# Kernel tuning notes

Hardware: AMD Instinct MI355X
Metric: run time of the kernel (lower is better)

Reference implementation:

```python
import jax, jax.numpy as jnp
import numpy as np

B, S, H, NH = 2, 2048, 1024, 16
DH = H // NH
FF = 4 * H
EPS = 1e-5


def setup_inputs() -> dict:
    key = jax.random.key(0)
    ks = jax.random.split(key, 16)
    sd = 0.02
    inp = {
        "x": jax.random.normal(ks[0], (B, S, H), dtype=jnp.float32),
        "Wq": jax.random.normal(ks[1], (H, H), dtype=jnp.float32) * sd,
        "bq": jnp.zeros((H,), jnp.float32),
        "Wk": jax.random.normal(ks[2], (H, H), dtype=jnp.float32) * sd,
        "bk": jnp.zeros((H,), jnp.float32),
        "Wv": jax.random.normal(ks[3], (H, H), dtype=jnp.float32) * sd,
        "bv": jnp.zeros((H,), jnp.float32),
        "Wo": jax.random.normal(ks[4], (H, H), dtype=jnp.float32) * sd,
        "bo": jnp.zeros((H,), jnp.float32),
        "W1": jax.random.normal(ks[5], (H, FF), dtype=jnp.float32) * sd,
        "b1": jnp.zeros((FF,), jnp.float32),
        "W2": jax.random.normal(ks[6], (FF, H), dtype=jnp.float32) * sd,
        "b2": jnp.zeros((H,), jnp.float32),
        "g1": jnp.ones((H,), jnp.float32),
        "be1": jnp.zeros((H,), jnp.float32),
        "g2": jnp.ones((H,), jnp.float32),
        "be2": jnp.zeros((H,), jnp.float32),
    }
    return inp


def _layernorm(x, g, b):
    mu = jnp.mean(x, axis=-1, keepdims=True)
    var = jnp.mean(jnp.square(x - mu), axis=-1, keepdims=True)
    return (x - mu) * jax.lax.rsqrt(var + EPS) * g + b


def _block(x, Wq, bq, Wk, bk, Wv, bv, Wo, bo, W1, b1, W2, b2, g1, be1, g2, be2):
    # pre-LN attention
    h = _layernorm(x, g1, be1)
    q = (h @ Wq + bq).reshape(B, S, NH, DH)
    k = (h @ Wk + bk).reshape(B, S, NH, DH)
    v = (h @ Wv + bv).reshape(B, S, NH, DH)
    scale = DH ** -0.5
    scores = jnp.einsum("bqhd,bkhd->bhqk", q, k) * scale  # [B,NH,S,S]
    causal = jnp.tril(jnp.ones((S, S), dtype=bool))
    scores = jnp.where(causal, scores, -jnp.inf)
    attn = jax.nn.softmax(scores, axis=-1)
    out = jnp.einsum("bhqk,bkhd->bqhd", attn, v).reshape(B, S, H)
    x = x + (out @ Wo + bo)
    # pre-LN FFN with exact GELU (torch nn.GELU default)
    h = _layernorm(x, g2, be2)
    h = jax.nn.gelu(h @ W1 + b1, approximate=False)
    return x + (h @ W2 + b2)


def reference(x, Wq, bq, Wk, bk, Wv, bv, Wo, bo, W1, b1, W2, b2, g1, be1, g2, be2):
    return _block(x, Wq, bq, Wk, bk, Wv, bv, Wo, bo, W1, b1, W2, b2, g1, be1, g2, be2)
```

## Files before the change

### kernel.cpp

```cpp
#include <hip/hip_runtime.h>
#include <cstdint>
#include <cstddef>

typedef unsigned short u16;
typedef __attribute__((ext_vector_type(8))) __bf16 bf16v8;
typedef __attribute__((ext_vector_type(8))) unsigned short u16x8;
typedef __attribute__((ext_vector_type(4))) float f32x4;

constexpr int Bc = 2, Sc = 2048, Hc = 1024, NHc = 16, DHc = 64, FFc = 4096;
constexpr int Mc = Bc * Sc;

__device__ __forceinline__ u16 f2bf(float f) {
  unsigned u = __builtin_bit_cast(unsigned, f);
  return (u16)((u + 0x7FFFu + ((u >> 16) & 1u)) >> 16);
}

__device__ __forceinline__ void gload_lds16(const void* g, void* l) {
  __builtin_amdgcn_global_load_lds(
      (const __attribute__((address_space(1))) unsigned*)(uintptr_t)g,
      (__attribute__((address_space(3))) unsigned*)(unsigned)(uintptr_t)l,
      16, 0, 0);
}

__global__ __launch_bounds__(256) void wconv_kernel(const float* __restrict__ W,
                                                    u16* __restrict__ Wt, int K, int N) {
  __shared__ float tile[64][65];
  const int n0 = blockIdx.x << 6, k0 = blockIdx.y << 6;
  const int t = threadIdx.x;
  const int col = t & 63, r0 = t >> 6;
#pragma unroll
  for (int i = 0; i < 16; ++i) {
    int r = (i << 2) + r0;
    tile[r][col] = W[(size_t)(k0 + r) * N + n0 + col];
  }
  __syncthreads();
#pragma unroll
  for (int i = 0; i < 16; ++i) {
    int n = (i << 2) + r0;
    Wt[(size_t)(n0 + n) * K + k0 + col] = f2bf(tile[col][n]);
  }
}

__global__ __launch_bounds__(256) void ln_kernel(const float* __restrict__ x,
                                                 const float* __restrict__ g,
                                                 const float* __restrict__ be,
                                                 u16* __restrict__ y) {
  const int row = blockIdx.x;
  const int t = threadIdx.x;
  const float4 v = ((const float4*)(x + (size_t)row * Hc))[t];
  float s1 = v.x + v.y + v.z + v.w;
  float s2 = v.x * v.x + v.y * v.y + v.z * v.z + v.w * v.w;
#pragma unroll
  for (int o = 32; o > 0; o >>= 1) {
    s1 += __shfl_xor(s1, o);
    s2 += __shfl_xor(s2, o);
  }
  __shared__ float r1[4], r2[4];
  const int wave = t >> 6, lane = t & 63;
  if (lane == 0) { r1[wave] = s1; r2[wave] = s2; }
  __syncthreads();
  s1 = r1[0] + r1[1] + r1[2] + r1[3];
  s2 = r2[0] + r2[1] + r2[2] + r2[3];
  const float mu = s1 * (1.f / Hc);
  const float var = s2 * (1.f / Hc) - mu * mu;
  const float rs = rsqrtf(var + 1e-5f);
  const float4 gv = ((const float4*)g)[t];
  const float4 bv = ((const float4*)be)[t];
  ushort4 ov;
  ov.x = f2bf((v.x - mu) * rs * gv.x + bv.x);
  ov.y = f2bf((v.y - mu) * rs * gv.y + bv.y);
  ov.z = f2bf((v.z - mu) * rs * gv.z + bv.z);
  ov.w = f2bf((v.w - mu) * rs * gv.w + bv.w);
  ((ushort4*)(y + (size_t)row * Hc))[t] = ov;
}

template <int EPI>
__global__ __launch_bounds__(256, 2) void gemm_kernel(
    const u16* __restrict__ A, const u16* __restrict__ Bt,
    const float* __restrict__ bias, const float* __restrict__ res,
    u16* __restrict__ outb, float* __restrict__ outf, float* __restrict__ outf2,
    int N, int Kext, int lda, int ldb, int koff) {
  __shared__ __align__(16) char smraw[32768];
  u16 (*As)[128][32] = (u16(*)[128][32])smraw;
  u16 (*Bs)[128][32] = (u16(*)[128][32])(smraw + 16384);
  float (*Cs)[16][132] = (float(*)[16][132])smraw;

  const int t = threadIdx.x;
  const int wave = t >> 6, lane = t & 63;
  const int bm = blockIdx.y, bn = blockIdx.x;
  const int kz = blockIdx.z;
  A += (size_t)kz * koff;
  Bt += (size_t)kz * koff;
  const int wm = wave >> 1, wn = wave & 1;
  const int fr = lane & 15, fk = (lane >> 4) << 3;

  f32x4 acc[4][4] = {};

  const int srow = (wave << 4) + (lane >> 2);
  const int scol = (lane & 3) << 3;
  const u16* Ag0 = A + (size_t)(bm * 128 + srow) * lda + scol;
  const u16* Ag1 = Ag0 + (size_t)64 * lda;
  const u16* Bg0 = Bt + (size_t)(bn * 128 + srow) * ldb + scol;
  const u16* Bg1 = Bg0 + (size_t)64 * ldb;

  const int nk = Kext >> 5;
  auto STAGE = [&](int buf, int k0) {
    gload_lds16(Ag0 + k0, &As[buf][wave << 4][0]);
    gload_lds16(Ag1 + k0, &As[buf][64 + (wave << 4)][0]);
    gload_lds16(Bg0 + k0, &Bs[buf][wave << 4][0]);
    gload_lds16(Bg1 + k0, &Bs[buf][64 + (wave << 4)][0]);
  };

  STAGE(0, 0);
  asm volatile("s_waitcnt vmcnt(0)" ::: "memory");
  __syncthreads();
  int cur = 0;
  for (int kt = 0; kt < nk; ++kt) {
    if (kt + 1 < nk) STAGE(cur ^ 1, (kt + 1) << 5);
    bf16v8 af[4], bfr[4];
#pragma unroll
    for (int i = 0; i < 4; ++i) af[i] = *(const bf16v8*)&As[cur][(wm << 6) + (i << 4) + fr][fk];
#pragma unroll
    for (int j = 0; j < 4; ++j) bfr[j] = *(const bf16v8*)&Bs[cur][(wn << 6) + (j << 4) + fr][fk];
#pragma unroll
    for (int i = 0; i < 4; ++i)
#pragma unroll
      for (int j = 0; j < 4; ++j)
        acc[i][j] = __builtin_amdgcn_mfma_f32_16x16x32_bf16(af[i], bfr[j], acc[i][j], 0, 0, 0);
    asm volatile("s_waitcnt vmcnt(0)" ::: "memory");
    __syncthreads();
    cur ^= 1;
  }

  const int cr = (lane >> 4) << 2, cc = lane & 15;
  const int b2 = t >> 7, u = t & 127, lr = u >> 3, c0 = (u & 7) << 4;
  float* fdst = (EPI == 3 && kz) ? outf2 : outf;

  for (int i = 0; i < 4; ++i) {
#pragma unroll
    for (int j = 0; j < 4; ++j) {
      int col = (wn << 6) + (j << 4) + cc;
      float bz = 0.f;
      if constexpr (EPI != 3) bz = bias[(bn << 7) + col];
#pragma unroll
      for (int r = 0; r < 4; ++r) Cs[wm][cr + r][col] = acc[i][j][r] + bz;
    }
    __syncthreads();
    {
      const float* crow = &Cs[b2][lr][c0];
      f32x4 v0 = *(const f32x4*)(crow);
      f32x4 v1 = *(const f32x4*)(crow + 4);
      f32x4 v2 = *(const f32x4*)(crow + 8);
      f32x4 v3 = *(const f32x4*)(crow + 12);
      const int grow = (bm << 7) + (b2 << 6) + (i << 4) + lr;
      const int gc = (bn << 7) + c0;
      const size_t base = (size_t)grow * N + gc;
      if constexpr (EPI == 0 || EPI == 1) {
        float vv[16];
#pragma unroll
        for (int k = 0; k < 4; ++k) { vv[k] = v0[k]; vv[4 + k] = v1[k]; vv[8 + k] = v2[k]; vv[12 + k] = v3[k]; }
        if constexpr (EPI == 1) {
#pragma unroll
          for (int k = 0; k < 16; ++k)
            vv[k] = 0.5f * vv[k] * (1.0f + erff(vv[k] * 0.70710678118654752f));
        }
        u16x8 o0, o1;
#pragma unroll
        for (int k = 0; k < 8; ++k) { o0[k] = f2bf(vv[k]); o1[k] = f2bf(vv[8 + k]); }
        *(u16x8*)&outb[base] = o0;
        *(u16x8*)&outb[base + 8] = o1;
      } else {
        if constexpr (EPI == 2) {
          const f32x4* rp = (const f32x4*)&res[base];
          v0 += rp[0]; v1 += rp[1]; v2 += rp[2]; v3 += rp[3];
        }
        f32x4* op = (f32x4*)&fdst[base];
        op[0] = v0; op[1] = v1; op[2] = v2; op[3] = v3;
      }
    }
    __syncthreads();
  }
}

__global__ __launch_bounds__(256, 2) void qkv_gemm_kernel(
    const u16* __restrict__ A, const u16* __restrict__ Bt,
    const float* __restrict__ bq, const float* __restrict__ bk,
    const float* __restrict__ bv,
    u16* __restrict__ Qb, u16* __restrict__ Kb, u16* __restrict__ Vtg) {
  constexpr int K = 1024;
  __shared__ __align__(16) char smraw[32768];
  u16 (*As)[128][32] = (u16(*)[128][32])smraw;
  u16 (*Bs)[128][32] = (u16(*)[128][32])(smraw + 16384);
  float (*Cs)[16][132] = (float(*)[16][132])smraw;

  const int t = threadIdx.x;
  const int wave = t >> 6, lane = t & 63;
  const int bm = blockIdx.y, bn = blockIdx.x;
  const int wm = wave >> 1, wn = wave & 1;
  const int fr = lane & 15, fk = (lane >> 4) << 3;
  const int seg = bn >> 3;

  f32x4 acc[4][4] = {};

  const int srow = (wave << 4) + (lane >> 2);
  const int scol = (lane & 3) << 3;
  const u16* Ag0 = A + (size_t)(bm * 128 + srow) * K + scol;
  const u16* Ag1 = Ag0 + (size_t)64 * K;
  const u16* Bg0 = Bt + (size_t)(bn * 128 + srow) * K + scol;
  const u16* Bg1 = Bg0 + (size_t)64 * K;

  const int nk = K >> 5;
  auto STAGE = [&](int buf, int k0) {
    gload_lds16(Ag0 + k0, &As[buf][wave << 4][0]);
    gload_lds16(Ag1 + k0, &As[buf][64 + (wave << 4)][0]);
    gload_lds16(Bg0 + k0, &Bs[buf][wave << 4][0]);
    gload_lds16(Bg1 + k0, &Bs[buf][64 + (wave << 4)][0]);
  };

  STAGE(0, 0);
  asm volatile("s_waitcnt vmcnt(0)" ::: "memory");
  __syncthreads();
  int cur = 0;
  for (int kt = 0; kt < nk; ++kt) {
    if (kt + 1 < nk) STAGE(cur ^ 1, (kt + 1) << 5);
    bf16v8 af[4], bfr[4];
#pragma unroll
    for (int i = 0; i < 4; ++i) af[i] = *(const bf16v8*)&As[cur][(wm << 6) + (i << 4) + fr][fk];
#pragma unroll
    for (int j = 0; j < 4; ++j) bfr[j] = *(const bf16v8*)&Bs[cur][(wn << 6) + (j << 4) + fr][fk];
#pragma unroll
    for (int i = 0; i < 4; ++i)
#pragma unroll
      for (int j = 0; j < 4; ++j)
        acc[i][j] = __builtin_amdgcn_mfma_f32_16x16x32_bf16(af[i], bfr[j], acc[i][j], 0, 0, 0);
    asm volatile("s_waitcnt vmcnt(0)" ::: "memory");
    __syncthreads();
    cur ^= 1;
  }

  const int cr = (lane >> 4) << 2, cc = lane & 15;
  const int b2 = t >> 7, u = t & 127, lr = u >> 3, c0 = (u & 7) << 4;
  const float* bp = (seg == 0) ? bq : (seg == 1) ? bk : bv;

  for (int i = 0; i < 4; ++i) {
#pragma unroll
    for (int j = 0; j < 4; ++j) {
      int col = (wn << 6) + (j << 4) + cc;
      float bz = bp[((bn << 7) + col) & 1023];
#pragma unroll
      for (int r = 0; r < 4; ++r) Cs[wm][cr + r][col] = acc[i][j][r] + bz;
    }
    __syncthreads();
    if (seg < 2) {
      const float* crow = &Cs[b2][lr][c0];
      f32x4 v0 = *(const f32x4*)(crow);
      f32x4 v1 = *(const f32x4*)(crow + 4);
      f32x4 v2 = *(const f32x4*)(crow + 8);
      f32x4 v3 = *(const f32x4*)(crow + 12);
      const int grow = (bm << 7) + (b2 << 6) + (i << 4) + lr;
      const int cn0 = (((bn & 7) << 7) + c0);
      u16* dst = (seg == 0) ? Qb : Kb;
      u16x8 o0, o1;
#pragma unroll
      for (int k = 0; k < 4; ++k) {
        o0[k] = f2bf(v0[k]); o0[4 + k] = f2bf(v1[k]);
        o1[k] = f2bf(v2[k]); o1[4 + k] = f2bf(v3[k]);
      }
      *(u16x8*)&dst[(size_t)grow * 1024 + cn0] = o0;
      *(u16x8*)&dst[(size_t)grow * 1024 + cn0 + 8] = o1;
    } else {
      const int cv = ((bn & 7) << 7) + u;
      const int h = cv >> 6, dh = cv & 63;
#pragma unroll
      for (int oct = 0; oct < 2; ++oct) {
        u16x8 o;
#pragma unroll
        for (int k = 0; k < 8; ++k) o[k] = f2bf(Cs[b2][(oct << 3) + k][u]);
        const int srow2 = (bm << 7) + (b2 << 6) + (i << 4) + (oct << 3);
        const int bb = srow2 >> 11, s = srow2 & 2047;
        size_t idx = ((size_t)(bb * 16 + h)) * (64 * 2048) + (size_t)dh * 2048 + s;
        *(u16x8*)&Vtg[idx] = o;
      }
    }
    __syncthreads();
  }
}

__global__ __launch_bounds__(256) void combine_kernel(float* __restrict__ out,
                                                      const float* __restrict__ p0,
                                                      const float* __restrict__ p1,
                                                      const float* __restrict__ bias) {
  const int i = blockIdx.x * 256 + threadIdx.x;
  f32x4 o = ((f32x4*)out)[i];
  f32x4 a = ((const f32x4*)p0)[i];
  f32x4 b = ((const f32x4*)p1)[i];
  const int col = (i << 2) & 1023;
  f32x4 bb = *(const f32x4*)&bias[col];
  o += a + b + bb;
  ((f32x4*)out)[i] = o;
}

__global__ __launch_bounds__(256, 2) void attn_kernel(const u16* __restrict__ Q,
                                                      const u16* __restrict__ Kb,
                                                      const u16* __restrict__ Vt,
                                                      u16* __restrict__ O) {
  constexpr float LOG2E = 1.4426950408889634f;
  const int bh = blockIdx.y;
  const int t = threadIdx.x, wave = t >> 6, lane = t & 63;
  const int fr = lane & 15, fk = (lane >> 4) << 3;

  __shared__ u16 Ks[64][72];
  __shared__ u16 Vs[64][72];
  __shared__ u16 Ps[4][16][72];

  const size_t base = ((size_t)(bh >> 4) * Sc) * Hc + (bh & 15) * DHc;
  const u16* Qp = Q + base;
  const u16* Kp = Kb + base;
  const u16* Vp = Vt + (size_t)bh * (64 * 2048);

  for (int half = 0; half < 2; ++half) {
    const int qt = half ? (31 - blockIdx.x) : blockIdx.x;
    const int q0 = qt << 6;

    const int qrow = q0 + (wave << 4) + fr;
    const bf16v8 qf0 = *(const bf16v8*)&Qp[(size_t)qrow * Hc + fk];
    const bf16v8 qf1 = *(const bf16v8*)&Qp[(size_t)qrow * Hc + 32 + fk];

    float m[4], l[4];
    f32x4 oacc[4] = {};
#pragma unroll
    for (int r = 0; r < 4; ++r) { m[r] = -INFINITY; l[r] = 0.f; }

    const int crow0 = q0 + (wave << 4) + ((lane >> 4) << 2);

    for (int kv0 = 0; kv0 < q0 + 64; kv0 += 64) {
      __syncthreads();
#pragma unroll
      for (int i = 0; i < 2; ++i) {
        int c = t + (i << 8);
        int r = c >> 3, co = (c & 7) << 3;
        *(u16x8*)&Ks[r][co] = *(const u16x8*)&Kp[(size_t)(kv0 + r) * Hc + co];
        *(u16x8*)&Vs[r][co] = *(const u16x8*)&Vp[(size_t)r * 2048 + kv0 + co];
      }
      __syncthreads();

      f32x4 sc[4];
#pragma unroll
      for (int c = 0; c < 4; ++c) {
        bf16v8 kf0 = *(const bf16v8*)&Ks[(c << 4) + fr][fk];
        bf16v8 kf1 = *(const bf16v8*)&Ks[(c << 4) + fr][32 + fk];
        f32x4 a = {0.f, 0.f, 0.f, 0.f};
        a = __builtin_amdgcn_mfma_f32_16x16x32_bf16(qf0, kf0, a, 0, 0, 0);
        a = __builtin_amdgcn_mfma_f32_16x16x32_bf16(qf1, kf1, a, 0, 0, 0);
        sc[c] = a;
      }
#pragma unroll
      for (int c = 0; c < 4; ++c)
#pragma unroll
        for (int r = 0; r < 4; ++r) sc[c][r] *= 0.125f;
      if (kv0 + 64 > q0) {
#pragma unroll
        for (int c = 0; c < 4; ++c)
#pragma unroll
          for (int r = 0; r < 4; ++r) {
            int kv = kv0 + (c << 4) + fr;
            if (kv > crow0 + r) sc[c][r] = -INFINITY;
          }
      }
      float pm[4];
#pragma unroll
      for (int r = 0; r < 4; ++r)
        pm[r] = fmaxf(fmaxf(sc[0][r], sc[1][r]), fmaxf(sc[2][r], sc[3][r]));
#pragma unroll
      for (int o = 1; o < 16; o <<= 1)
#pragma unroll
        for (int r = 0; r < 4; ++r) pm[r] = fmaxf(pm[r], __shfl_xor(pm[r], o));
      float alpha[4];
#pragma unroll
      for (int r = 0; r < 4; ++r) {
        float mn = fmaxf(m[r], pm[r]);
        alpha[r] = exp2f((m[r] - mn) * LOG2E);
        m[r] = mn;
      }
      float ps[4] = {0.f, 0.f, 0.f, 0.f};
#pragma unroll
      for (int c = 0; c < 4; ++c)
#pragma unroll
        for (int r = 0; r < 4; ++r) {
          float p = exp2f((sc[c][r] - m[r]) * LOG2E);
          sc[c][r] = p;
          ps[r] += p;
        }
#pragma unroll
      for (int o = 1; o < 16; o <<= 1)
#pragma unroll
        for (int r = 0; r < 4; ++r) ps[r] += __shfl_xor(ps[r], o);
#pragma unroll
      for (int r = 0; r < 4; ++r) l[r] = l[r] * alpha[r] + ps[r];

#pragma unroll
      for (int c = 0; c < 4; ++c)
#pragma unroll
        for (int r = 0; r < 4; ++r)
          Ps[wave][((lane >> 4) << 2) + r][(c << 4) + fr] = f2bf(sc[c][r]);
#pragma unroll
      for (int f = 0; f < 4; ++f)
#pragma unroll
        for (int r = 0; r < 4; ++r) oacc[f][r] *= alpha[r];

      const bf16v8 pa0 = *(const bf16v8*)&Ps[wave][fr][fk];
      const bf16v8 pa1 = *(const bf16v8*)&Ps[wave][fr][32 + fk];
#pragma unroll
      for (int f = 0; f < 4; ++f) {
        bf16v8 vf0 = *(const bf16v8*)&Vs[(f << 4) + fr][fk];
        bf16v8 vf1 = *(const bf16v8*)&Vs[(f << 4) + fr][32 + fk];
        oacc[f] = __builtin_amdgcn_mfma_f32_16x16x32_bf16(pa0, vf0, oacc[f], 0, 0, 0);
        oacc[f] = __builtin_amdgcn_mfma_f32_16x16x32_bf16(pa1, vf1, oacc[f], 0, 0, 0);
      }
    }
#pragma unroll
    for (int r = 0; r < 4; ++r) {
      float inv = 1.0f / l[r];
      int row = crow0 + r;
#pragma unroll
      for (int f = 0; f < 4; ++f)
        O[base + (size_t)row * Hc + (f << 4) + fr] = f2bf(oacc[f][r] * inv);
    }
    __syncthreads();
  }
}

extern "C" void kernel_launch(void* const* d_in, const int* in_sizes, int n_in,
                              void* d_out, int out_size, void* d_ws, size_t ws_size,
                              hipStream_t stream) {
  const float* x  = (const float*)d_in[0];
  const float* Wq = (const float*)d_in[1];
  const float* bq = (const float*)d_in[2];
  const float* Wk = (const float*)d_in[3];
  const float* bk = (const float*)d_in[4];
  const float* Wv = (const float*)d_in[5];
  const float* bv = (const float*)d_in[6];
  const float* Wo = (const float*)d_in[7];
  const float* bo = (const float*)d_in[8];
  const float* W1 = (const float*)d_in[9];
  const float* b1 = (const float*)d_in[10];
  const float* W2 = (const float*)d_in[11];
  const float* b2 = (const float*)d_in[12];
  const float* g1 = (const float*)d_in[13];
  const float* be1 = (const float*)d_in[14];
  const float* g2 = (const float*)d_in[15];
  const float* be2 = (const float*)d_in[16];
  float* out = (float*)d_out;

  char* ws = (char*)d_ws;
  const size_t MB = 1024 * 1024;
  u16* wqkv = (u16*)(ws + 0 * MB);
  u16* wo   = (u16*)(ws + 6 * MB);
  u16* w1   = (u16*)(ws + 8 * MB);
  u16* w2   = (u16*)(ws + 16 * MB);
  u16* lnb  = (u16*)(ws + 24 * MB);
  u16* Qb   = (u16*)(ws + 32 * MB);
  u16* Kb   = (u16*)(ws + 40 * MB);
  u16* Vtg  = (u16*)(ws + 48 * MB);
  u16* Ob   = (u16*)(ws + 56 * MB);
  u16* H1   = (u16*)(ws + 32 * MB);
  float* p0 = (float*)(ws + 64 * MB);
  float* p1 = (float*)(ws + 0 * MB);

  dim3 blk(256);
  wconv_kernel<<<dim3(16, 16), blk, 0, stream>>>(Wq, wqkv, 1024, 1024);
  wconv_kernel<<<dim3(16, 16), blk, 0, stream>>>(Wk, wqkv + (size_t)1024 * 1024, 1024, 1024);
  wconv_kernel<<<dim3(16, 16), blk, 0, stream>>>(Wv, wqkv + (size_t)2048 * 1024, 1024, 1024);
  wconv_kernel<<<dim3(16, 16), blk, 0, stream>>>(Wo, wo, 1024, 1024);
  wconv_kernel<<<dim3(64, 16), blk, 0, stream>>>(W1, w1, 1024, 4096);
  wconv_kernel<<<dim3(16, 64), blk, 0, stream>>>(W2, w2, 4096, 1024);

  ln_kernel<<<Mc, blk, 0, stream>>>(x, g1, be1, lnb);

  qkv_gemm_kernel<<<dim3(24, 32), blk, 0, stream>>>(lnb, wqkv, bq, bk, bv, Qb, Kb, Vtg);

  attn_kernel<<<dim3(16, 32), blk, 0, stream>>>(Qb, Kb, Vtg, Ob);

  gemm_kernel<2><<<dim3(8, 32), blk, 0, stream>>>(Ob, wo, bo, x, nullptr, out, nullptr,
                                                  1024, 1024, 1024, 1024, 0);

  ln_kernel<<<Mc, blk, 0, stream>>>(out, g2, be2, lnb);

  gemm_kernel<1><<<dim3(32, 32), blk, 0, stream>>>(lnb, w1, b1, nullptr, H1, nullptr, nullptr,
                                                   4096, 1024, 1024, 1024, 0);

  gemm_kernel<3><<<dim3(8, 32, 2), blk, 0, stream>>>(H1, w2, nullptr, nullptr, nullptr, p0, p1,
                                                     1024, 2048, 4096, 4096, 2048);
  combine_kernel<<<dim3(4096), blk, 0, stream>>>(out, p0, p1, b2);
}
```

Before: 297.6 us.

## Add XCD-aware block swizzle, MFMA priority, and double-buffered attention KV loads

Flattens the GEMM and attention grids to 1D and remaps block IDs so consecutive tiles land on the same XCD, aiming for better L2 reuse. Wraps the MFMA loops in s_setprio to favour matrix issue. Attention now double-buffers K/V tiles through registers so global loads overlap compute, folds the 0.125 scale into the exp2 constant via fma, and raises the occupancy hint to 3 blocks. The extra LDS and register use may limit occupancy.

Result: faster. 285.4 us (-4.1%).

```diff
diff --git a/kernel.cpp b/kernel.cpp
--- a/kernel.cpp
+++ b/kernel.cpp
@@ -13,6 +13,11 @@
 __device__ __forceinline__ u16 f2bf(float f) {
   unsigned u = __builtin_bit_cast(unsigned, f);
   return (u16)((u + 0x7FFFu + ((u >> 16) & 1u)) >> 16);
+}
+
+__device__ __forceinline__ int xcd_swz(int bid, int n) {
+  const int q = n >> 3;
+  return (bid & 7) * q + (bid >> 3);
 }
 
 __device__ __forceinline__ void gload_lds16(const void* g, void* l) {
@@ -79,7 +84,7 @@
     const u16* __restrict__ A, const u16* __restrict__ Bt,
     const float* __restrict__ bias, const float* __restrict__ res,
     u16* __restrict__ outb, float* __restrict__ outf, float* __restrict__ outf2,
-    int N, int Kext, int lda, int ldb, int koff) {
+    int N, int Kext, int lda, int ldb, int koff, int nx) {
   __shared__ __align__(16) char smraw[32768];
   u16 (*As)[128][32] = (u16(*)[128][32])smraw;
   u16 (*Bs)[128][32] = (u16(*)[128][32])(smraw + 16384);
@@ -87,7 +92,8 @@
 
   const int t = threadIdx.x;
   const int wave = t >> 6, lane = t & 63;
-  const int bm = blockIdx.y, bn = blockIdx.x;
+  const int pid = xcd_swz(blockIdx.x, gridDim.x);
+  const int bn = pid % nx, bm = pid / nx;
   const int kz = blockIdx.z;
   A += (size_t)kz * koff;
   Bt += (size_t)kz * koff;
@@ -122,11 +128,13 @@
     for (int i = 0; i < 4; ++i) af[i] = *(const bf16v8*)&As[cur][(wm << 6) + (i << 4) + fr][fk];
 #pragma unroll
     for (int j = 0; j < 4; ++j) bfr[j] = *(const bf16v8*)&Bs[cur][(wn << 6) + (j << 4) + fr][fk];
+    __builtin_amdgcn_s_setprio(1);
 #pragma unroll
     for (int i = 0; i < 4; ++i)
 #pragma unroll
       for (int j = 0; j < 4; ++j)
         acc[i][j] = __builtin_amdgcn_mfma_f32_16x16x32_bf16(af[i], bfr[j], acc[i][j], 0, 0, 0);
+    __builtin_amdgcn_s_setprio(0);
     asm volatile("s_waitcnt vmcnt(0)" ::: "memory");
     __syncthreads();
     cur ^= 1;
@@ -195,7 +203,8 @@
 
   const int t = threadIdx.x;
   const int wave = t >> 6, lane = t & 63;
-  const int bm = blockIdx.y, bn = blockIdx.x;
+  const int pid = xcd_swz(blockIdx.x, 768);
+  const int bn = pid % 24, bm = pid / 24;
   const int wm = wave >> 1, wn = wave & 1;
   const int fr = lane & 15, fk = (lane >> 4) << 3;
   const int seg = bn >> 3;
@@ -228,11 +237,13 @@
     for (int i = 0; i < 4; ++i) af[i] = *(const bf16v8*)&As[cur][(wm << 6) + (i << 4) + fr][fk];
 #pragma unroll
     for (int j = 0; j < 4; ++j) bfr[j] = *(const bf16v8*)&Bs[cur][(wn << 6) + (j << 4) + fr][fk];
+    __builtin_amdgcn_s_setprio(1);
 #pragma unroll
     for (int i = 0; i < 4; ++i)
 #pragma unroll
       for (int j = 0; j < 4; ++j)
         acc[i][j] = __builtin_amdgcn_mfma_f32_16x16x32_bf16(af[i], bfr[j], acc[i][j], 0, 0, 0);
+    __builtin_amdgcn_s_setprio(0);
     asm volatile("s_waitcnt vmcnt(0)" ::: "memory");
     __syncthreads();
     cur ^= 1;
@@ -300,17 +311,18 @@
   ((f32x4*)out)[i] = o;
 }
 
-__global__ __launch_bounds__(256, 2) void attn_kernel(const u16* __restrict__ Q,
+__global__ __launch_bounds__(256, 3) void attn_kernel(const u16* __restrict__ Q,
                                                       const u16* __restrict__ Kb,
                                                       const u16* __restrict__ Vt,
                                                       u16* __restrict__ O) {
-  constexpr float LOG2E = 1.4426950408889634f;
-  const int bh = blockIdx.y;
+  constexpr float CS = 0.18033688011112042f;
+  const int pid = xcd_swz(blockIdx.x, 512);
+  const int bx = pid & 15, bh = pid >> 4;
   const int t = threadIdx.x, wave = t >> 6, lane = t & 63;
   const int fr = lane & 15, fk = (lane >> 4) << 3;
 
-  __shared__ u16 Ks[64][72];
-  __shared__ u16 Vs[64][72];
+  __shared__ u16 Ks[2][64][72];
+  __shared__ u16 Vs[2][64][72];
   __shared__ u16 Ps[4][16][72];
 
   const size_t base = ((size_t)(bh >> 4) * Sc) * Hc + (bh & 15) * DHc;
@@ -318,9 +330,13 @@
   const u16* Kp = Kb + base;
   const u16* Vp = Vt + (size_t)bh * (64 * 2048);
 
+  const int r_st = t >> 3;
+  const int co_st = (t & 7) << 3;
+
   for (int half = 0; half < 2; ++half) {
-    const int qt = half ? (31 - blockIdx.x) : blockIdx.x;
+    const int qt = half ? (31 - bx) : bx;
     const int q0 = qt << 6;
+    const int nt = qt + 1;
 
     const int qrow = q0 + (wave << 4) + fr;
     const bf16v8 qf0 = *(const bf16v8*)&Qp[(size_t)qrow * Hc + fk];
@@ -333,31 +349,42 @@
 
     const int crow0 = q0 + (wave << 4) + ((lane >> 4) << 2);
 
-    for (int kv0 = 0; kv0 < q0 + 64; kv0 += 64) {
-      __syncthreads();
-#pragma unroll
-      for (int i = 0; i < 2; ++i) {
-        int c = t + (i << 8);
-        int r = c >> 3, co = (c & 7) << 3;
-        *(u16x8*)&Ks[r][co] = *(const u16x8*)&Kp[(size_t)(kv0 + r) * Hc + co];
-        *(u16x8*)&Vs[r][co] = *(const u16x8*)&Vp[(size_t)r * 2048 + kv0 + co];
-      }
-      __syncthreads();
+    u16x8 rk0, rk1, rv0, rv1;
+    auto LD = [&](int kv0) {
+      rk0 = *(const u16x8*)&Kp[(size_t)(kv0 + r_st) * Hc + co_st];
+      rk1 = *(const u16x8*)&Kp[(size_t)(kv0 + 32 + r_st) * Hc + co_st];
+      rv0 = *(const u16x8*)&Vp[(size_t)r_st * 2048 + kv0 + co_st];
+      rv1 = *(const u16x8*)&Vp[(size_t)(32 + r_st) * 2048 + kv0 + co_st];
+    };
+    auto WR = [&](int buf) {
+      *(u16x8*)&Ks[buf][r_st][co_st] = rk0;
+      *(u16x8*)&Ks[buf][32 + r_st][co_st] = rk1;
+      *(u16x8*)&Vs[buf][r_st][co_st] = rv0;
+      *(u16x8*)&Vs[buf][32 + r_st][co_st] = rv1;
+    };
+
+    LD(0);
+    WR(0);
+    __syncthreads();
+    int cur = 0;
+    for (int it = 0; it < nt; ++it) {
+      const int kv0 = it << 6;
+      const bool hasnext = (it + 1 < nt);
+      if (hasnext) LD(kv0 + 64);
 
       f32x4 sc[4];
+      __builtin_amdgcn_s_setprio(1);
 #pragma unroll
       for (int c = 0; c < 4; ++c) {
-        bf16v8 kf0 = *(const bf16v8*)&Ks[(c << 4) + fr][fk];
-        bf16v8 kf1 = *(const bf16v8*)&Ks[(c << 4) + fr][32 + fk];
+        bf16v8 kf0 = *(const bf16v8*)&Ks[cur][(c << 4) + fr][fk];
+        bf16v8 kf1 = *(const bf16v8*)&Ks[cur][(c << 4) + fr][32 + fk];
         f32x4 a = {0.f, 0.f, 0.f, 0.f};
         a = __builtin_amdgcn_mfma_f32_16x16x32_bf16(qf0, kf0, a, 0, 0, 0);
         a = __builtin_amdgcn_mfma_f32_16x16x32_bf16(qf1, kf1, a, 0, 0, 0);
         sc[c] = a;
       }
-#pragma unroll
-      for (int c = 0; c < 4; ++c)
-#pragma unroll
-        for (int r = 0; r < 4; ++r) sc[c][r] *= 0.125f;
+      __builtin_amdgcn_s_setprio(0);
+
       if (kv0 + 64 > q0) {
 #pragma unroll
         for (int c = 0; c < 4; ++c)
@@ -375,19 +402,20 @@
       for (int o = 1; o < 16; o <<= 1)
 #pragma unroll
         for (int r = 0; r < 4; ++r) pm[r] = fmaxf(pm[r], __shfl_xor(pm[r], o));
-      float alpha[4];
+      float alpha[4], nm[4];
 #pragma unroll
       for (int r = 0; r < 4; ++r) {
-        float mn = fmaxf(m[r], pm[r]);
-        alpha[r] = exp2f((m[r] - mn) * LOG2E);
-        m[r] = mn;
+        float mx = fmaxf(m[r], pm[r]);
+        alpha[r] = exp2f((m[r] - mx) * CS);
+        m[r] = mx;
+        nm[r] = -mx * CS;
       }
       float ps[4] = {0.f, 0.f, 0.f, 0.f};
 #pragma unroll
       for (int c = 0; c < 4; ++c)
 #pragma unroll
         for (int r = 0; r < 4; ++r) {
-          float p = exp2f((sc[c][r] - m[r]) * LOG2E);
+          float p = exp2f(fmaf(sc[c][r], CS, nm[r]));
           sc[c][r] = p;
           ps[r] += p;
         }
@@ -410,13 +438,19 @@
 
       const bf16v8 pa0 = *(const bf16v8*)&Ps[wave][fr][fk];
       const bf16v8 pa1 = *(const bf16v8*)&Ps[wave][fr][32 + fk];
+      __builtin_amdgcn_s_setprio(1);
 #pragma unroll
       for (int f = 0; f < 4; ++f) {
-        bf16v8 vf0 = *(const bf16v8*)&Vs[(f << 4) + fr][fk];
-        bf16v8 vf1 = *(const bf16v8*)&Vs[(f << 4) + fr][32 + fk];
+        bf16v8 vf0 = *(const bf16v8*)&Vs[cur][(f << 4) + fr][fk];
+        bf16v8 vf1 = *(const bf16v8*)&Vs[cur][(f << 4) + fr][32 + fk];
         oacc[f] = __builtin_amdgcn_mfma_f32_16x16x32_bf16(pa0, vf0, oacc[f], 0, 0, 0);
         oacc[f] = __builtin_amdgcn_mfma_f32_16x16x32_bf16(pa1, vf1, oacc[f], 0, 0, 0);
       }
+      __builtin_amdgcn_s_setprio(0);
+
+      if (hasnext) WR(cur ^ 1);
+      __syncthreads();
+      cur ^= 1;
     }
 #pragma unroll
     for (int r = 0; r < 4; ++r) {
@@ -477,19 +511,19 @@
 
   ln_kernel<<<Mc, blk, 0, stream>>>(x, g1, be1, lnb);
 
-  qkv_gemm_kernel<<<dim3(24, 32), blk, 0, stream>>>(lnb, wqkv, bq, bk, bv, Qb, Kb, Vtg);
-
-  attn_kernel<<<dim3(16, 32), blk, 0, stream>>>(Qb, Kb, Vtg, Ob);
-
-  gemm_kernel<2><<<dim3(8, 32), blk, 0, stream>>>(Ob, wo, bo, x, nullptr, out, nullptr,
-                                                  1024, 1024, 1024, 1024, 0);
+  qkv_gemm_kernel<<<dim3(768), blk, 0, stream>>>(lnb, wqkv, bq, bk, bv, Qb, Kb, Vtg);
+
+  attn_kernel<<<dim3(512), blk, 0, stream>>>(Qb, Kb, Vtg, Ob);
+
+  gemm_kernel<2><<<dim3(256), blk, 0, stream>>>(Ob, wo, bo, x, nullptr, out, nullptr,
+                                                1024, 1024, 1024, 1024, 0, 8);
 
   ln_kernel<<<Mc, blk, 0, stream>>>(out, g2, be2, lnb);
 
-  gemm_kernel<1><<<dim3(32, 32), blk, 0, stream>>>(lnb, w1, b1, nullptr, H1, nullptr, nullptr,
-                                                   4096, 1024, 1024, 1024, 0);
-
-  gemm_kernel<3><<<dim3(8, 32, 2), blk, 0, stream>>>(H1, w2, nullptr, nullptr, nullptr, p0, p1,
-                                                     1024, 2048, 4096, 4096, 2048);
+  gemm_kernel<1><<<dim3(1024), blk, 0, stream>>>(lnb, w1, b1, nullptr, H1, nullptr, nullptr,
+                                                 4096, 1024, 1024, 1024, 0, 32);
+
+  gemm_kernel<3><<<dim3(256, 1, 2), blk, 0, stream>>>(H1, w2, nullptr, nullptr, nullptr, p0, p1,
+                                                      1024, 2048, 4096, 4096, 2048, 8);
   combine_kernel<<<dim3(4096), blk, 0, stream>>>(out, p0, p1, b2);
 }
```
